# Performance work log

Hardware: AMD Instinct MI355X
Metric: run time of the kernel (lower is better)

The kernel has to match this reference:

```python
import jax, jax.numpy as jnp
import numpy as np

POOL = (4000, 4000, 4000)
N_GO = 12000
N_GENES = 20000
IN_F = 8
F = 64
B = 8
D_ATT = 5
L_DIM = 16
N_LAST = 4000
EPS = 1e-5


def _seg(v, ids, n):
    # v: [B, E, ...] -> segment-sum over axis 1
    return jax.vmap(lambda a: jax.ops.segment_sum(a, ids, num_segments=n))(v)


def _ln_nodes(x, g, b):
    # torch does LayerNorm(N) on x.permute(0,2,1): normalize over the NODE axis
    mu = x.mean(axis=1, keepdims=True)
    var = x.var(axis=1, keepdims=True)
    return (x - mu) * jax.lax.rsqrt(var + EPS) * g[None, :, None] + b[None, :, None]


def _bn(x, g, b):
    # BatchNorm1d, training-mode statistics (biased var); channel axis = 1
    if x.ndim == 2:
        mu = x.mean(axis=0)
        var = x.var(axis=0)
        return (x - mu) * jax.lax.rsqrt(var + EPS) * g + b
    mu = x.mean(axis=(0, 2), keepdims=True)
    var = x.var(axis=(0, 2), keepdims=True)
    return (x - mu) * jax.lax.rsqrt(var + EPS) * g[None, :, None] + b[None, :, None]


def _enc(x, src, dst, n, w_inc, w_s, w_att_in, w_att_s, g, b):
    x_in = x @ w_inc.T                 # [B,n,F]
    x_s = x @ w_s.T
    f1 = w_inc.shape[0]
    # W_att_in([x_src; x_dst]) == x_src @ W[:, :f1].T + x_dst @ W[:, f1:].T (GAT trick)
    a_src = x_in @ w_att_in[0, :f1]    # [B,n]
    a_dst = x_in @ w_att_in[0, f1:]
    v = jnp.exp(jnp.tanh(a_src[:, src] + a_dst[:, dst]))   # [B,E]
    vn = v / _seg(v, src, n)[:, src]                        # row-normalized attention
    x_incoming = _seg(vn[:, :, None] * x_in[:, dst, :], src, n)
    v_s = jax.nn.sigmoid(x_s @ w_att_s[0])                  # [B,n]
    out = x_incoming + x_s * v_s[:, :, None]
    return jax.nn.relu(_ln_nodes(out, g, b))


def _dec(x, src, dst, n_rows, offset, w_out, w_sout, g, b):
    x_out = x @ w_out.T
    x_s = x @ w_sout.T
    deg = jax.ops.segment_sum(jnp.ones(src.shape, x.dtype), src, num_segments=n_rows)
    v = 1.0 / deg[src]                                      # [E]
    x_outgoing = _seg(v[None, :, None] * x_out[:, dst, :], src, n_rows)
    out = x_outgoing.at[:, offset:, :].add(x_s)
    return jax.nn.relu(_ln_nodes(out, g, b))


def _forward(data, t, t_D,
             w_inc0, w_inc1, w_s0, w_s1, w_att_in0, w_att_in1, w_att_s0, w_att_s1,
             gb_g0, gb_b0, gb_g1, gb_b1,
             w_out0, w_out1, w_sout0, w_sout1,
             gbd_g0, gbd_b0, gbd_g1, gbd_b1,
             catt_w, catt_bn_g, catt_bn_b,
             conc_w, b_bn_g, b_bn_b,
             concd_w, bd_bn_g, bd_bn_b,
             lat_w1, lat_bn1_g, lat_bn1_b, lat_w2, lat_bn2_g, lat_bn2_b,
             Ag_row, Ag_col,
             enc_src0, enc_dst0, enc_src1, enc_dst1,
             dec_src0, dec_dst0, dec_src1, dec_dst1):
    # initial SNP->GO sparse embedding, one sparse matrix per input channel
    gathered = data[:, Ag_col]                         # [B,nnz]
    msg0 = gathered[:, :, None] * t.T[None, :, :]      # [B,nnz,IN_F]
    x = _seg(msg0, Ag_row, N_GO)                       # [B,N_GO,IN_F]

    # encoder (attention GCN + pooling)
    x = _enc(x, enc_src0, enc_dst0, N_GO, w_inc0, w_s0, w_att_in0, w_att_s0, gb_g0, gb_b0)
    x = x[:, POOL[0]:, :]
    x = _enc(x, enc_src1, enc_dst1, N_GO - POOL[0], w_inc1, w_s1, w_att_in1, w_att_s1, gb_g1, gb_b1)
    x = x[:, POOL[1]:, :]                              # [B,N_LAST,F]

    atten_out = jax.nn.relu(_bn(x @ catt_w.T, catt_bn_g, catt_bn_b))   # [B,N_LAST,D_ATT]
    inp_out = jax.nn.relu(_bn((x @ conc_w.T)[..., 0], b_bn_g, b_bn_b)) # [B,N_LAST]

    # decoder (degree-normalized unpooling)
    x = _dec(x, dec_src0, dec_dst0, POOL[1] + POOL[2], POOL[1], w_out0, w_sout0, gbd_g0, gbd_b0)
    x = _dec(x, dec_src1, dec_dst1, N_GO, POOL[0], w_out1, w_sout1, gbd_g1, gbd_b1)

    out_D = jax.nn.relu(_bn((x @ concd_w.T)[..., 0], bd_bn_g, bd_bn_b))  # [B,N_GO]
    x_D = _seg(out_D[:, Ag_row] * t_D[None, :], Ag_col, N_GENES)          # [B,N_GENES]

    h = jax.nn.relu(_bn(inp_out @ lat_w1.T, lat_bn1_g, lat_bn1_b))
    latent = jax.nn.relu(_bn(h @ lat_w2.T, lat_bn2_g, lat_bn2_b))         # [B,L_DIM]
    return latent, x_D, atten_out


def setup_inputs():
    rng = np.random.default_rng(0)
    # GO-GO adjacency edges (row-major unique, like coalesce)
    e = np.unique(rng.integers(0, N_GO, 144000).astype(np.int64) * N_GO
                  + rng.integers(0, N_GO, 144000))
    r = (e // N_GO).astype(np.int32)
    c = (e % N_GO).astype(np.int32)
    p0, p1 = POOL[0], POOL[0] + POOL[1]
    m = (r >= p0) & (c >= p0)
    enc_src1, enc_dst1 = r[m] - p0, c[m] - p0
    ti, tj = c, r                                  # edges of A.T
    m0 = (ti >= p0) & (tj >= p1)
    dec_src0, dec_dst0 = ti[m0] - p0, tj[m0] - p1
    m1 = tj >= p0
    dec_src1, dec_dst1 = ti[m1], tj[m1] - p0
    # gene <-> GO incidence
    eg = np.unique(rng.integers(0, N_GO, 240000).astype(np.int64) * N_GENES
                   + rng.integers(0, N_GENES, 240000))
    Ag_row = (eg // N_GENES).astype(np.int32)
    Ag_col = (eg % N_GENES).astype(np.int32)
    nnz = Ag_row.shape[0]

    ks = iter(jax.random.split(jax.random.key(0), 40))

    def nrm(shape, s=0.05):
        return jax.random.normal(next(ks), shape, jnp.float32) * s

    return {
        'data': nrm((B, N_GENES), 1.0),
        't': 1.0 + nrm((IN_F, nnz), 0.1),
        't_D': 1.0 + nrm((nnz,), 0.1),
        'w_inc0': nrm((F, IN_F)), 'w_inc1': nrm((F, F)),
        'w_s0': nrm((F, IN_F)), 'w_s1': nrm((F, F)),
        'w_att_in0': nrm((1, 2 * F)), 'w_att_in1': nrm((1, 2 * F)),
        'w_att_s0': nrm((1, F)), 'w_att_s1': nrm((1, F)),
        'gb_g0': jnp.ones(N_GO), 'gb_b0': jnp.zeros(N_GO),
        'gb_g1': jnp.ones(N_GO - p0), 'gb_b1': jnp.zeros(N_GO - p0),
        'w_out0': nrm((F, F)), 'w_out1': nrm((IN_F, F)),
        'w_sout0': nrm((F, F)), 'w_sout1': nrm((IN_F, F)),
        'gbd_g0': jnp.ones(POOL[1] + POOL[2]), 'gbd_b0': jnp.zeros(POOL[1] + POOL[2]),
        'gbd_g1': jnp.ones(N_GO), 'gbd_b1': jnp.zeros(N_GO),
        'catt_w': nrm((D_ATT, F)), 'catt_bn_g': jnp.ones(N_LAST), 'catt_bn_b': jnp.zeros(N_LAST),
        'conc_w': nrm((1, F)), 'b_bn_g': jnp.ones(N_LAST), 'b_bn_b': jnp.zeros(N_LAST),
        'concd_w': nrm((1, IN_F)), 'bd_bn_g': jnp.ones(N_GO), 'bd_bn_b': jnp.zeros(N_GO),
        'lat_w1': nrm((32, N_LAST)), 'lat_bn1_g': jnp.ones(32), 'lat_bn1_b': jnp.zeros(32),
        'lat_w2': nrm((L_DIM, 32)), 'lat_bn2_g': jnp.ones(L_DIM), 'lat_bn2_b': jnp.zeros(L_DIM),
        'Ag_row': jnp.asarray(Ag_row), 'Ag_col': jnp.asarray(Ag_col),
        'enc_src0': jnp.asarray(r), 'enc_dst0': jnp.asarray(c),
        'enc_src1': jnp.asarray(enc_src1), 'enc_dst1': jnp.asarray(enc_dst1),
        'dec_src0': jnp.asarray(dec_src0), 'dec_dst0': jnp.asarray(dec_dst0),
        'dec_src1': jnp.asarray(dec_src1), 'dec_dst1': jnp.asarray(dec_dst1),
    }


def reference(data, t, t_D,
              w_inc0, w_inc1, w_s0, w_s1, w_att_in0, w_att_in1, w_att_s0, w_att_s1,
              gb_g0, gb_b0, gb_g1, gb_b1,
              w_out0, w_out1, w_sout0, w_sout1,
              gbd_g0, gbd_b0, gbd_g1, gbd_b1,
              catt_w, catt_bn_g, catt_bn_b,
              conc_w, b_bn_g, b_bn_b,
              concd_w, bd_bn_g, bd_bn_b,
              lat_w1, lat_bn1_g, lat_bn1_b, lat_w2, lat_bn2_g, lat_bn2_b,
              Ag_row, Ag_col,
              enc_src0, enc_dst0, enc_src1, enc_dst1,
              dec_src0, dec_dst0, dec_src1, dec_dst1):
    return _forward(data, t, t_D,
                    w_inc0, w_inc1, w_s0, w_s1, w_att_in0, w_att_in1, w_att_s0, w_att_s1,
                    gb_g0, gb_b0, gb_g1, gb_b1,
                    w_out0, w_out1, w_sout0, w_sout1,
                    gbd_g0, gbd_b0, gbd_g1, gbd_b1,
                    catt_w, catt_bn_g, catt_bn_b,
                    conc_w, b_bn_g, b_bn_b,
                    concd_w, bd_bn_g, bd_bn_b,
                    lat_w1, lat_bn1_g, lat_bn1_b, lat_w2, lat_bn2_g, lat_bn2_b,
                    Ag_row, Ag_col,
                    enc_src0, enc_dst0, enc_src1, enc_dst1,
                    dec_src0, dec_dst0, dec_src1, dec_dst1)
```

## Files before the change

### kernel.cpp

```cpp
#include <hip/hip_runtime.h>
#include <math.h>

#define BB 8
#define N_GO 12000
#define N_GENES 20000
#define IN_F 8
#define FF 64
#define D_ATT 5
#define L_DIM 16
#define N_LAST 4000
#define P0_ 4000
#define EPSF 1e-5f

__global__ void k_bounds_bs(const int* __restrict__ src, int* __restrict__ rs,
                            int* __restrict__ re, int E, int n) {
    int r = blockIdx.x * 256 + threadIdx.x;
    if (r >= n) return;
    int lo = 0, hi = E;
    while (lo < hi) { int m = (lo + hi) >> 1; if (src[m] < r) lo = m + 1; else hi = m; }
    rs[r] = lo;
    int lo2 = lo, hi2 = E;
    while (lo2 < hi2) { int m = (lo2 + hi2) >> 1; if (src[m] < r + 1) lo2 = m + 1; else hi2 = m; }
    re[r] = lo2;
}

__global__ void k_tr_data(const float* __restrict__ data, float* __restrict__ dataT) {
    int idx = blockIdx.x * 256 + threadIdx.x;
    if (idx >= N_GENES * BB) return;
    int g = idx >> 3, b = idx & 7;
    dataT[idx] = data[b * N_GENES + g];
}

__global__ void k_gene2go_w(const float* __restrict__ dataT, const float* __restrict__ t,
                            const int* __restrict__ col, const int* __restrict__ rs,
                            const int* __restrict__ re, float* __restrict__ x0, int nnz) {
    int wid = blockIdx.x * 4 + (threadIdx.x >> 6);
    if (wid >= N_GO) return;
    int lane = threadIdx.x & 63;
    int f = lane & 7, eo = lane >> 3;
    int e0 = rs[wid], e1 = re[wid];
    float acc[BB];
#pragma unroll
    for (int b = 0; b < BB; b++) acc[b] = 0.f;
    for (int e = e0; e < e1; e += 8) {
        int ee = e + eo;
        bool ok = ee < e1;
        int ec = ok ? ee : (e1 - 1);
        int c = col[ec];
        float tv = ok ? t[(size_t)f * nnz + ee] : 0.f;
        const float4* dt = (const float4*)(dataT + (size_t)c * 8);
        float4 d0 = dt[0], d1 = dt[1];
        acc[0] += tv * d0.x; acc[1] += tv * d0.y; acc[2] += tv * d0.z; acc[3] += tv * d0.w;
        acc[4] += tv * d1.x; acc[5] += tv * d1.y; acc[6] += tv * d1.z; acc[7] += tv * d1.w;
    }
#pragma unroll
    for (int b = 0; b < BB; b++) {
        acc[b] += __shfl_xor(acc[b], 8);
        acc[b] += __shfl_xor(acc[b], 16);
        acc[b] += __shfl_xor(acc[b], 32);
    }
    if (lane < IN_F) {
#pragma unroll
        for (int b = 0; b < BB; b++)
            x0[((size_t)b * N_GO + wid) * IN_F + lane] = acc[b];
    }
}

template<bool SCAL>
__global__ __launch_bounds__(256, 2)
void k_linear2_att8(const float* __restrict__ X, const float* __restrict__ W1,
                    const float* __restrict__ W2, const float* __restrict__ watt,
                    const float* __restrict__ ws, float* __restrict__ Y1,
                    float* __restrict__ Y2, float* __restrict__ ASRC,
                    float* __restrict__ ADST,
                    int n_nodes, long xbs, int xoff, int total_waves) {
    __shared__ float w1s[IN_F * 65];
    __shared__ float w2s[IN_F * 65];
    int lane = threadIdx.x & 63;
    for (int i = threadIdx.x; i < IN_F * FF; i += 256) {
        int fo = i >> 3, k = i & 7;
        w1s[k * 65 + fo] = W1[i];
        w2s[k * 65 + fo] = W2[i];
    }
    __syncthreads();
    float w1r[IN_F], w2r[IN_F];
#pragma unroll
    for (int k = 0; k < IN_F; k++) {
        w1r[k] = w1s[k * 65 + lane];
        w2r[k] = w2s[k * 65 + lane];
        asm volatile("" : "+v"(w1r[k]));
        asm volatile("" : "+v"(w2r[k]));
    }
    float wa = 0.f, wb = 0.f, wc = 0.f;
    if (SCAL) { wa = watt[lane]; wb = watt[FF + lane]; wc = ws[lane]; }
    int wid = blockIdx.x * 4 + (threadIdx.x >> 6);
    for (int n = wid; n < n_nodes; n += total_waves) {
        for (int b = 0; b < BB; b++) {
            const float* xr = X + (size_t)b * xbs + (size_t)(n + xoff) * IN_F;
            float4 x0 = *(const float4*)xr, x1 = *(const float4*)(xr + 4);
            float a1 = x0.x * w1r[0] + x0.y * w1r[1] + x0.z * w1r[2] + x0.w * w1r[3]
                     + x1.x * w1r[4] + x1.y * w1r[5] + x1.z * w1r[6] + x1.w * w1r[7];
            float a2 = x0.x * w2r[0] + x0.y * w2r[1] + x0.z * w2r[2] + x0.w * w2r[3]
                     + x1.x * w2r[4] + x1.y * w2r[5] + x1.z * w2r[6] + x1.w * w2r[7];
            Y1[((size_t)b * n_nodes + n) * FF + lane] = a1;
            if (SCAL) {
                float s0 = a1 * wa, s1 = a1 * wb, s2 = a2 * wc;
                for (int m = 1; m < 64; m <<= 1) {
                    s0 += __shfl_xor(s0, m);
                    s1 += __shfl_xor(s1, m);
                    s2 += __shfl_xor(s2, m);
                }
                float vs = 1.f / (1.f + expf(-s2));
                Y2[((size_t)b * n_nodes + n) * FF + lane] = a2 * vs;
                if (lane == 0) {
                    ASRC[b * n_nodes + n] = s0;
                    ADST[b * n_nodes + n] = s1;
                }
            } else {
                Y2[((size_t)b * n_nodes + n) * FF + lane] = a2;
            }
        }
    }
}

template<bool SCAL>
__global__ __launch_bounds__(256, 1)
void k_lin64d(const float* __restrict__ X, const float* __restrict__ W1,
              const float* __restrict__ W2, const float* __restrict__ watt,
              const float* __restrict__ ws, float* __restrict__ Y1,
              float* __restrict__ Y2, float* __restrict__ ASRC,
              float* __restrict__ ADST,
              int n_nodes, long xbs, int xoff, int total_waves) {
    __shared__ float w1s[FF * 65];
    __shared__ float w2s[FF * 65];
    int lane = threadIdx.x & 63;
    for (int i = threadIdx.x; i < FF * FF; i += 256) {
        int fo = i >> 6, k = i & 63;
        w1s[fo * 65 + k] = W1[i];
        w2s[fo * 65 + k] = W2[i];
    }
    __syncthreads();
    float w1r[FF], w2r[FF];
#pragma unroll
    for (int k = 0; k < FF; k++) {
        w1r[k] = w1s[lane * 65 + k];
        w2r[k] = w2s[lane * 65 + k];
        asm volatile("" : "+v"(w1r[k]));
        asm volatile("" : "+v"(w2r[k]));
    }
    float wa = 0.f, wb = 0.f, wc = 0.f;
    if (SCAL) { wa = watt[lane]; wb = watt[FF + lane]; wc = ws[lane]; }
    int wid = blockIdx.x * 4 + (threadIdx.x >> 6);
    for (int n = wid; n < n_nodes; n += total_waves) {
        for (int b = 0; b < BB; b++) {
            const float* xr = X + (size_t)b * xbs + (size_t)(n + xoff) * FF;
            float a1 = 0.f, a2 = 0.f;
#pragma unroll
            for (int k = 0; k < FF; k += 4) {
                float4 x = *(const float4*)(xr + k);
                a1 += x.x * w1r[k] + x.y * w1r[k + 1] + x.z * w1r[k + 2] + x.w * w1r[k + 3];
                a2 += x.x * w2r[k] + x.y * w2r[k + 1] + x.z * w2r[k + 2] + x.w * w2r[k + 3];
            }
            Y1[((size_t)b * n_nodes + n) * FF + lane] = a1;
            if (SCAL) {
                float s0 = a1 * wa, s1 = a1 * wb, s2 = a2 * wc;
                for (int m = 1; m < 64; m <<= 1) {
                    s0 += __shfl_xor(s0, m);
                    s1 += __shfl_xor(s1, m);
                    s2 += __shfl_xor(s2, m);
                }
                float vs = 1.f / (1.f + expf(-s2));
                Y2[((size_t)b * n_nodes + n) * FF + lane] = a2 * vs;
                if (lane == 0) {
                    ASRC[b * n_nodes + n] = s0;
                    ADST[b * n_nodes + n] = s1;
                }
            } else {
                Y2[((size_t)b * n_nodes + n) * FF + lane] = a2;
            }
        }
    }
}

__global__ __launch_bounds__(256, 1)
void k_lin8d(const float* __restrict__ X, const float* __restrict__ W1,
             const float* __restrict__ W2, float* __restrict__ Y1,
             float* __restrict__ Y2, int n_nodes, long xbs, int xoff,
             int total_waves) {
    __shared__ float w1s[IN_F * 65];
    __shared__ float w2s[IN_F * 65];
    int lane = threadIdx.x & 63;
    for (int i = threadIdx.x; i < IN_F * FF; i += 256) {
        int fo = i >> 6, k = i & 63;
        w1s[fo * 65 + k] = W1[i];
        w2s[fo * 65 + k] = W2[i];
    }
    __syncthreads();
    int of = lane & 7;
    int slot = lane >> 3;
    float w1r[FF], w2r[FF];
#pragma unroll
    for (int k = 0; k < FF; k++) {
        w1r[k] = w1s[of * 65 + k];
        w2r[k] = w2s[of * 65 + k];
        asm volatile("" : "+v"(w1r[k]));
        asm volatile("" : "+v"(w2r[k]));
    }
    int wid = blockIdx.x * 4 + (threadIdx.x >> 6);
    for (long n0 = (long)wid * 8; n0 < n_nodes; n0 += (long)total_waves * 8) {
        int n = (int)n0 + slot;
        bool ok = (n < n_nodes);
        int nn = ok ? n : (n_nodes - 1);
        for (int b = 0; b < BB; b++) {
            const float* xr = X + (size_t)b * xbs + (size_t)(nn + xoff) * FF;
            float a1 = 0.f, a2 = 0.f;
#pragma unroll
            for (int k = 0; k < FF; k += 4) {
                float4 x = *(const float4*)(xr + k);
                a1 += x.x * w1r[k] + x.y * w1r[k + 1] + x.z * w1r[k + 2] + x.w * w1r[k + 3];
                a2 += x.x * w2r[k] + x.y * w2r[k + 1] + x.z * w2r[k + 2] + x.w * w2r[k + 3];
            }
            if (ok) {
                Y1[((size_t)b * n_nodes + n) * IN_F + of] = a1;
                Y2[((size_t)b * n_nodes + n) * IN_F + of] = a2;
            }
        }
    }
}

__global__ void k_edge_v(const float* __restrict__ a_src, const float* __restrict__ a_dst,
                         const int* __restrict__ src, const int* __restrict__ dst,
                         float* __restrict__ v, int E, int n_nodes) {
    int e = blockIdx.x * 256 + threadIdx.x;
    if (e >= E) return;
    int b = blockIdx.y;
    v[(size_t)b * E + e] = expf(tanhf(a_src[b * n_nodes + src[e]] + a_dst[b * n_nodes + dst[e]]));
}

__global__ void k_agg_enc_f(const float* __restrict__ Xin, const float* __restrict__ Xs,
                            const float* __restrict__ EDGEV,
                            const int* __restrict__ dst, const int* __restrict__ rs,
                            const int* __restrict__ re, float* __restrict__ Out,
                            float* __restrict__ sums, int n_nodes, int E, int nblk) {
    int b = blockIdx.x & 7;
    int wid = threadIdx.x >> 6;
    int lane = threadIdx.x & 63;
    const float* Xb  = Xin + (size_t)b * n_nodes * FF;
    const float* Xsb = Xs  + (size_t)b * n_nodes * FF;
    const float* vv  = EDGEV + (size_t)b * E;
    float s1 = 0.f, s2 = 0.f;
    for (int r = (blockIdx.x >> 3) * 4 + wid; r < n_nodes; r += nblk * 4) {
        int e0 = rs[r], e1 = re[r];
        float sv0 = 0.f, sv1 = 0.f, sv2 = 0.f, sv3 = 0.f;
        float acc0 = 0.f, acc1 = 0.f, acc2 = 0.f, acc3 = 0.f;
        int e = e0;
        for (; e + 3 < e1; e += 4) {
            int d0 = dst[e], d1 = dst[e + 1], d2 = dst[e + 2], d3 = dst[e + 3];
            float v0 = vv[e], v1 = vv[e + 1], v2 = vv[e + 2], v3 = vv[e + 3];
            sv0 += v0; sv1 += v1; sv2 += v2; sv3 += v3;
            acc0 += v0 * Xb[(size_t)d0 * FF + lane];
            acc1 += v1 * Xb[(size_t)d1 * FF + lane];
            acc2 += v2 * Xb[(size_t)d2 * FF + lane];
            acc3 += v3 * Xb[(size_t)d3 * FF + lane];
        }
        for (; e < e1; e++) {
            int d0 = dst[e];
            float v0 = vv[e];
            sv0 += v0;
            acc0 += v0 * Xb[(size_t)d0 * FF + lane];
        }
        float sv = (sv0 + sv1) + (sv2 + sv3);
        float acc = (acc0 + acc1) + (acc2 + acc3);
        float o = (e1 > e0) ? acc / sv : 0.f;
        o += Xsb[(size_t)r * FF + lane];
        Out[((size_t)b * n_nodes + r) * FF + lane] = o;
        s1 += o; s2 += o * o;
    }
    __shared__ float sh1[4][64], sh2[4][64];
    sh1[wid][lane] = s1; sh2[wid][lane] = s2;
    __syncthreads();
    if (wid == 0) {
        float a = sh1[0][lane] + sh1[1][lane] + sh1[2][lane] + sh1[3][lane];
        float c = sh2[0][lane] + sh2[1][lane] + sh2[2][lane] + sh2[3][lane];
        atomicAdd(&sums[(b * FF + lane) * 2],     a);
        atomicAdd(&sums[(b * FF + lane) * 2 + 1], c);
    }
}

__global__ void k_ln_stats(const float* __restrict__ X, float* __restrict__ sums,
                           int n_nodes, int Fdim, int npb) {
    int b = blockIdx.y;
    int f = threadIdx.x & (Fdim - 1);
    int nl = threadIdx.x / Fdim;
    int stride = 256 / Fdim;
    int n0 = blockIdx.x * npb;
    int n1 = n0 + npb; if (n1 > n_nodes) n1 = n_nodes;
    const float* xb = X + (size_t)b * n_nodes * Fdim;
    float s1 = 0.f, s2 = 0.f;
    for (int n = n0 + nl; n < n1; n += stride) {
        float x = xb[(size_t)n * Fdim + f];
        s1 += x; s2 += x * x;
    }
    __shared__ float sh1[256], sh2[256];
    sh1[threadIdx.x] = s1; sh2[threadIdx.x] = s2;
    __syncthreads();
    for (int o = 128; o >= Fdim; o >>= 1) {
        if (threadIdx.x < o) { sh1[threadIdx.x] += sh1[threadIdx.x + o]; sh2[threadIdx.x] += sh2[threadIdx.x + o]; }
        __syncthreads();
    }
    if (threadIdx.x < Fdim) {
        atomicAdd(&sums[(b * Fdim + threadIdx.x) * 2],     sh1[threadIdx.x]);
        atomicAdd(&sums[(b * Fdim + threadIdx.x) * 2 + 1], sh2[threadIdx.x]);
    }
}

__global__ void k_ln_apply_relu(const float* __restrict__ X, const float* __restrict__ sums,
                                const float* __restrict__ g, const float* __restrict__ bb,
                                float* __restrict__ Y, int n_nodes, int Fdim) {
    long idx = (long)blockIdx.x * 256 + threadIdx.x;
    if (idx >= (long)n_nodes * Fdim) return;
    int b = blockIdx.y;
    int n = (int)(idx / Fdim);
    int f = (int)(idx % Fdim);
    float s1 = sums[(b * Fdim + f) * 2], s2 = sums[(b * Fdim + f) * 2 + 1];
    float mu = s1 / n_nodes;
    float var = s2 / n_nodes - mu * mu;
    float rs = rsqrtf(var + EPSF);
    size_t o = (size_t)b * n_nodes * Fdim + idx;
    float y = (X[o] - mu) * rs * g[n] + bb[n];
    Y[o] = fmaxf(y, 0.f);
}

__global__ void k_deg_i(const int* __restrict__ src, int* __restrict__ deg, int E) {
    int e = blockIdx.x * 256 + threadIdx.x;
    if (e < E) atomicAdd(&deg[src[e]], 1);
}

__global__ void k_scan(const int* __restrict__ deg, int* __restrict__ rsd,
                       int* __restrict__ cursor, int n) {
    __shared__ int part[1024];
    int t = threadIdx.x;
    int chunk = (n + 1023) >> 10;
    int s0 = t * chunk, s1 = s0 + chunk; if (s1 > n) s1 = n;
    int s = 0;
    for (int i = s0; i < s1 && i < n; i++) s += deg[i];
    part[t] = s;
    __syncthreads();
    for (int o = 1; o < 1024; o <<= 1) {
        int v = (t >= o) ? part[t - o] : 0;
        __syncthreads();
        part[t] += v;
        __syncthreads();
    }
    int base = (t == 0) ? 0 : part[t - 1];
    for (int i = s0; i < s1 && i < n; i++) {
        rsd[i] = base; cursor[i] = base;
        base += deg[i];
    }
    if (t == 1023) rsd[n] = part[1023];
}

__global__ void k_scatter(const int* __restrict__ src, const int* __restrict__ dst,
                          int* __restrict__ cursor, int* __restrict__ csrd, int E) {
    int e = blockIdx.x * 256 + threadIdx.x;
    if (e >= E) return;
    int pos = atomicAdd(&cursor[src[e]], 1);
    csrd[pos] = dst[e];
}

__global__ void k_scatter2(const int* __restrict__ key, const int* __restrict__ row,
                           const float* __restrict__ tD, int* __restrict__ cursor,
                           int* __restrict__ csrr, float* __restrict__ csrt, int E) {
    int e = blockIdx.x * 256 + threadIdx.x;
    if (e >= E) return;
    int pos = atomicAdd(&cursor[key[e]], 1);
    csrr[pos] = row[e];
    csrt[pos] = tD[e];
}

__global__ void k_xd_g(const float* __restrict__ outD, const int* __restrict__ rsg,
                       const int* __restrict__ csrr, const float* __restrict__ csrt,
                       float* __restrict__ xD) {
    int g = blockIdx.x * 4 + (threadIdx.x >> 6);
    if (g >= N_GENES) return;
    int lane = threadIdx.x & 63;
    int b = lane & 7, slot = lane >> 3;
    int e0 = rsg[g], e1 = rsg[g + 1];
    float acc = 0.f;
    for (int e = e0 + slot; e < e1; e += 8)
        acc += csrt[e] * outD[(size_t)b * N_GO + csrr[e]];
    acc += __shfl_xor(acc, 8);
    acc += __shfl_xor(acc, 16);
    acc += __shfl_xor(acc, 32);
    if (lane < BB)
        xD[(size_t)b * N_GENES + g] = acc;
}

__global__ void k_agg_dec64(const float* __restrict__ Xout, const float* __restrict__ Xs,
                            const int* __restrict__ rsd, const int* __restrict__ csrd,
                            float* __restrict__ Out, float* __restrict__ sums,
                            int n_rows, int n_in, int offset, int nblk) {
    int b = blockIdx.x & 7;
    int wid = threadIdx.x >> 6;
    int lane = threadIdx.x & 63;
    const float* Xb = Xout + (size_t)b * n_in * FF;
    int nxs = n_rows - offset;
    const float* Xsb = Xs + (size_t)b * nxs * FF;
    float s1 = 0.f, s2 = 0.f;
    for (int r = (blockIdx.x >> 3) * 4 + wid; r < n_rows; r += nblk * 4) {
        int e0 = rsd[r], e1 = rsd[r + 1];
        float acc0 = 0.f, acc1 = 0.f, acc2 = 0.f, acc3 = 0.f;
        int e = e0;
        for (; e + 3 < e1; e += 4) {
            acc0 += Xb[(size_t)csrd[e] * FF + lane];
            acc1 += Xb[(size_t)csrd[e + 1] * FF + lane];
            acc2 += Xb[(size_t)csrd[e + 2] * FF + lane];
            acc3 += Xb[(size_t)csrd[e + 3] * FF + lane];
        }
        for (; e < e1; e++) acc0 += Xb[(size_t)csrd[e] * FF + lane];
        float acc = (acc0 + acc1) + (acc2 + acc3);
        float o = (e1 > e0) ? acc / (float)(e1 - e0) : 0.f;
        if (r >= offset)
            o += Xsb[(size_t)(r - offset) * FF + lane];
        Out[((size_t)b * n_rows + r) * FF + lane] = o;
        s1 += o; s2 += o * o;
    }
    __shared__ float sh1[4][64], sh2[4][64];
    sh1[wid][lane] = s1; sh2[wid][lane] = s2;
    __syncthreads();
    if (wid == 0) {
        float a = sh1[0][lane] + sh1[1][lane] + sh1[2][lane] + sh1[3][lane];
        float c = sh2[0][lane] + sh2[1][lane] + sh2[2][lane] + sh2[3][lane];
        atomicAdd(&sums[(b * FF + lane) * 2],     a);
        atomicAdd(&sums[(b * FF + lane) * 2 + 1], c);
    }
}

__global__ void k_agg_dec8(const float* __restrict__ Xout, const float* __restrict__ Xs,
                           const int* __restrict__ rsd, const int* __restrict__ csrd,
                           float* __restrict__ Out, int n_rows, int n_in, int offset) {
    int r = blockIdx.x * 4 + (threadIdx.x >> 6);
    if (r >= n_rows) return;
    int lane = threadIdx.x & 63;
    int f = lane & 7, slot = lane >> 3;
    int e0 = rsd[r], e1 = rsd[r + 1];
    float acc[BB];
#pragma unroll
    for (int b = 0; b < BB; b++) acc[b] = 0.f;
    for (int e = e0 + slot; e < e1; e += 8) {
        int d = csrd[e];
#pragma unroll
        for (int b = 0; b < BB; b++)
            acc[b] += Xout[((size_t)b * n_in + d) * IN_F + f];
    }
#pragma unroll
    for (int b = 0; b < BB; b++) {
        acc[b] += __shfl_xor(acc[b], 8);
        acc[b] += __shfl_xor(acc[b], 16);
        acc[b] += __shfl_xor(acc[b], 32);
    }
    float coef = (e1 > e0) ? 1.f / (float)(e1 - e0) : 0.f;
    int nxs = n_rows - offset;
    if (lane < IN_F) {
#pragma unroll
        for (int b = 0; b < BB; b++) {
            float o = acc[b] * coef;
            if (r >= offset)
                o += Xs[((size_t)b * nxs + (r - offset)) * IN_F + lane];
            Out[((size_t)b * n_rows + r) * IN_F + lane] = o;
        }
    }
}

__global__ void k_heads(const float* __restrict__ X, const float* __restrict__ Wa,
                        const float* __restrict__ wc, const float* __restrict__ ga,
                        const float* __restrict__ ba, const float* __restrict__ gc,
                        const float* __restrict__ bc, float* __restrict__ ATT,
                        float* __restrict__ INP, long xbs, int xoff) {
    int i = blockIdx.x * 4 + (threadIdx.x >> 6);
    if (i >= N_LAST) return;
    int lane = threadIdx.x & 63;
    float w0 = Wa[0 * FF + lane], w1 = Wa[1 * FF + lane], w2 = Wa[2 * FF + lane];
    float w3 = Wa[3 * FF + lane], w4 = Wa[4 * FF + lane];
    float wcv = wc[lane];
    float y[BB][D_ATT], yc[BB];
    float s1 = 0.f, s2 = 0.f;
#pragma unroll
    for (int b = 0; b < BB; b++) {
        float x = X[(size_t)b * xbs + (size_t)(i + xoff) * FF + lane];
        float p0 = x * w0, p1 = x * w1, p2 = x * w2, p3 = x * w3, p4 = x * w4, pc = x * wcv;
        for (int m = 1; m < 64; m <<= 1) {
            p0 += __shfl_xor(p0, m); p1 += __shfl_xor(p1, m); p2 += __shfl_xor(p2, m);
            p3 += __shfl_xor(p3, m); p4 += __shfl_xor(p4, m); pc += __shfl_xor(pc, m);
        }
        y[b][0] = p0; y[b][1] = p1; y[b][2] = p2; y[b][3] = p3; y[b][4] = p4;
        yc[b] = pc;
        s1 += p0 + p1 + p2 + p3 + p4;
        s2 += p0 * p0 + p1 * p1 + p2 * p2 + p3 * p3 + p4 * p4;
    }
    const float cnt = (float)(BB * D_ATT);
    float mu = s1 / cnt, var = s2 / cnt - mu * mu;
    float rsv = rsqrtf(var + EPSF);
    float gg = ga[i], bv = ba[i];
#pragma unroll
    for (int b = 0; b < BB; b++) {
        float yv = lane == 0 ? y[b][0] : lane == 1 ? y[b][1] : lane == 2 ? y[b][2]
                 : lane == 3 ? y[b][3] : y[b][4];
        if (lane < D_ATT)
            ATT[((size_t)b * N_LAST + i) * D_ATT + lane] = fmaxf((yv - mu) * rsv * gg + bv, 0.f);
    }
    float c1 = 0.f, c2 = 0.f;
#pragma unroll
    for (int b = 0; b < BB; b++) { c1 += yc[b]; c2 += yc[b] * yc[b]; }
    float muc = c1 / BB, varc = c2 / BB - muc * muc;
    float rc = rsqrtf(varc + EPSF);
    float ggc = gc[i], bvc = bc[i];
    if (lane < BB) {
        float v = lane == 0 ? yc[0] : lane == 1 ? yc[1] : lane == 2 ? yc[2] : lane == 3 ? yc[3]
                : lane == 4 ? yc[4] : lane == 5 ? yc[5] : lane == 6 ? yc[6] : yc[7];
        INP[(size_t)lane * N_LAST + i] = fmaxf((v - muc) * rc * ggc + bvc, 0.f);
    }
}

template<int FIN>
__global__ void k_head_scalar(const float* __restrict__ X, const float* __restrict__ w,
                              const float* __restrict__ g, const float* __restrict__ bb,
                              float* __restrict__ Z, int n_nodes, long xbs, int xoff) {
    int i = blockIdx.x * 256 + threadIdx.x;
    if (i >= n_nodes) return;
    float y[BB];
    float s1 = 0.f, s2 = 0.f;
    const float4* wr = (const float4*)w;
    for (int b = 0; b < BB; b++) {
        const float4* xr = (const float4*)(X + (size_t)b * xbs + (size_t)(i + xoff) * FIN);
        float acc = 0.f;
#pragma unroll
        for (int q = 0; q < FIN / 4; q++) {
            float4 x = xr[q], u = wr[q];
            acc += x.x * u.x + x.y * u.y + x.z * u.z + x.w * u.w;
        }
        y[b] = acc; s1 += acc; s2 += acc * acc;
    }
    float mu = s1 / BB, var = s2 / BB - mu * mu;
    float rs = rsqrtf(var + EPSF);
    float gg = g[i], bv = bb[i];
    for (int b = 0; b < BB; b++)
        Z[(size_t)b * n_nodes + i] = fmaxf((y[b] - mu) * rs * gg + bv, 0.f);
}

__global__ void k_lat1(const float* __restrict__ INP, const float* __restrict__ W,
                       const float* __restrict__ g, const float* __restrict__ bb,
                       float* __restrict__ H1R) {
    int j = blockIdx.x;
    int w = threadIdx.x >> 6;
    int lane = threadIdx.x & 63;
    const float* xr = INP + (size_t)w * N_LAST;
    const float* wr = W + (size_t)j * N_LAST;
    float s = 0.f;
    for (int k = lane; k < N_LAST; k += 64) s += xr[k] * wr[k];
    for (int o = 32; o > 0; o >>= 1) s += __shfl_down(s, o);
    __shared__ float sh[BB];
    if (lane == 0) sh[w] = s;
    __syncthreads();
    if (threadIdx.x < BB) {
        float s1 = 0.f, s2 = 0.f;
        for (int q = 0; q < BB; q++) { float y = sh[q]; s1 += y; s2 += y * y; }
        float mu = s1 / BB, var = s2 / BB - mu * mu;
        float rs = rsqrtf(var + EPSF);
        H1R[threadIdx.x * 32 + j] = fmaxf((sh[threadIdx.x] - mu) * rs * g[j] + bb[j], 0.f);
    }
}

__global__ void k_lat2(const float* __restrict__ H1R, const float* __restrict__ W2,
                       const float* __restrict__ g, const float* __restrict__ bb,
                       float* __restrict__ out_lat) {
    int b = threadIdx.x >> 4, j = threadIdx.x & 15;
    float acc = 0.f;
    for (int k = 0; k < 32; k++) acc += H1R[b * 32 + k] * W2[j * 32 + k];
    __shared__ float sh[128];
    sh[threadIdx.x] = acc;
    __syncthreads();
    float s1 = 0.f, s2 = 0.f;
    for (int q = 0; q < BB; q++) { float y = sh[q * 16 + j]; s1 += y; s2 += y * y; }
    float mu = s1 / BB, var = s2 / BB - mu * mu;
    float rs = rsqrtf(var + EPSF);
    out_lat[b * 16 + j] = fmaxf((acc - mu) * rs * g[j] + bb[j], 0.f);
}

extern "C" void kernel_launch(void* const* d_in, const int* in_sizes, int n_in,
                              void* d_out, int out_size, void* d_ws, size_t ws_size,
                              hipStream_t stream) {
    const float* data      = (const float*)d_in[0];
    const float* t         = (const float*)d_in[1];
    const float* t_D       = (const float*)d_in[2];
    const float* w_inc0    = (const float*)d_in[3];
    const float* w_inc1    = (const float*)d_in[4];
    const float* w_s0      = (const float*)d_in[5];
    const float* w_s1      = (const float*)d_in[6];
    const float* w_att_in0 = (const float*)d_in[7];
    const float* w_att_in1 = (const float*)d_in[8];
    const float* w_att_s0  = (const float*)d_in[9];
    const float* w_att_s1  = (const float*)d_in[10];
    const float* gb_g0     = (const float*)d_in[11];
    const float* gb_b0     = (const float*)d_in[12];
    const float* gb_g1     = (const float*)d_in[13];
    const float* gb_b1     = (const float*)d_in[14];
    const float* w_out0    = (const float*)d_in[15];
    const float* w_out1    = (const float*)d_in[16];
    const float* w_sout0   = (const float*)d_in[17];
    const float* w_sout1   = (const float*)d_in[18];
    const float* gbd_g0    = (const float*)d_in[19];
    const float* gbd_b0    = (const float*)d_in[20];
    const float* gbd_g1    = (const float*)d_in[21];
    const float* gbd_b1    = (const float*)d_in[22];
    const float* catt_w    = (const float*)d_in[23];
    const float* catt_bn_g = (const float*)d_in[24];
    const float* catt_bn_b = (const float*)d_in[25];
    const float* conc_w    = (const float*)d_in[26];
    const float* b_bn_g    = (const float*)d_in[27];
    const float* b_bn_b    = (const float*)d_in[28];
    const float* concd_w   = (const float*)d_in[29];
    const float* bd_bn_g   = (const float*)d_in[30];
    const float* bd_bn_b   = (const float*)d_in[31];
    const float* lat_w1    = (const float*)d_in[32];
    const float* lat_bn1_g = (const float*)d_in[33];
    const float* lat_bn1_b = (const float*)d_in[34];
    const float* lat_w2    = (const float*)d_in[35];
    const float* lat_bn2_g = (const float*)d_in[36];
    const float* lat_bn2_b = (const float*)d_in[37];
    const int* Ag_row   = (const int*)d_in[38];
    const int* Ag_col   = (const int*)d_in[39];
    const int* enc_src0 = (const int*)d_in[40];
    const int* enc_dst0 = (const int*)d_in[41];
    const int* enc_src1 = (const int*)d_in[42];
    const int* enc_dst1 = (const int*)d_in[43];
    const int* dec_src0 = (const int*)d_in[44];
    const int* dec_dst0 = (const int*)d_in[45];
    const int* dec_src1 = (const int*)d_in[46];
    const int* dec_dst1 = (const int*)d_in[47];

    const int nnz = in_sizes[2];
    const int E0  = in_sizes[40];
    const int E1  = in_sizes[42];
    const int ED0 = in_sizes[44];
    const int ED1 = in_sizes[46];
    int EDMAX = (ED0 > ED1 ? ED0 : ED1);
    if (nnz > EDMAX) EDMAX = nnz;

    char* wsb = (char*)d_ws;
    size_t off = 0;
    auto alloc = [&](size_t bytes) -> void* {
        void* p = wsb + off;
        off += (bytes + 255) & ~(size_t)255;
        return p;
    };
    const size_t ARENA = (size_t)BB * N_GO * FF;
    float* P0 = (float*)alloc(ARENA * 4);
    float* P1 = (float*)alloc(ARENA * 4);
    float* P2 = (float*)alloc(ARENA * 4);
    float* P3 = (float*)alloc(ARENA * 4);
    float* EDGEV = (float*)alloc((size_t)BB * E0 * 4);
    float* ASRC = (float*)alloc((size_t)BB * N_GO * 4);
    float* ADST = (float*)alloc((size_t)BB * N_GO * 4);
    float* SUMS = (float*)alloc(2 * BB * FF * 4);
    float* INP  = (float*)alloc((size_t)BB * N_LAST * 4);
    float* OUTD = (float*)alloc((size_t)BB * N_GO * 4);
    float* H1R  = (float*)alloc(BB * 32 * 4);
    float* DATAT = (float*)alloc((size_t)N_GENES * BB * 4);
    int* RS   = (int*)alloc(N_GO * 4);
    int* RE   = (int*)alloc(N_GO * 4);
    int* DEGI = (int*)alloc(N_GENES * 4);
    int* RSD  = (int*)alloc((N_GENES + 1) * 4);
    int* CURS = (int*)alloc(N_GENES * 4);
    int* CSRD = (int*)alloc((size_t)EDMAX * 4);
    float* CSRT = (float*)alloc((size_t)nnz * 4);

    float* out_lat = (float*)d_out;
    float* out_xd  = out_lat + BB * L_DIM;
    float* out_att = out_xd + (size_t)BB * N_GENES;

    dim3 blk(256);
    auto g1 = [](long n) { return dim3((unsigned)((n + 255) / 256)); };
    auto g2 = [](long n, int y) { return dim3((unsigned)((n + 255) / 256), (unsigned)y); };
    auto gw = [](int n) { return dim3((unsigned)((n + 3) / 4)); };
    const int LNB = 1024;
    const int LWAVES = LNB * 4;
    const int ANB = 256;
    const int N1 = N_GO - P0_;

    k_tr_data<<<g1(N_GENES * BB), blk, 0, stream>>>(data, DATAT);
    k_bounds_bs<<<g1(N_GO), blk, 0, stream>>>(Ag_row, RS, RE, nnz, N_GO);
    k_gene2go_w<<<gw(N_GO), blk, 0, stream>>>(DATAT, t, Ag_col, RS, RE, P0, nnz);

    k_linear2_att8<true><<<dim3(LNB), blk, 0, stream>>>(P0, w_inc0, w_s0, w_att_in0, w_att_s0,
        P1, P2, ASRC, ADST, N_GO, (long)N_GO * IN_F, 0, LWAVES);
    k_bounds_bs<<<g1(N_GO), blk, 0, stream>>>(enc_src0, RS, RE, E0, N_GO);
    k_edge_v<<<g2(E0, BB), blk, 0, stream>>>(ASRC, ADST, enc_src0, enc_dst0, EDGEV, E0, N_GO);
    hipMemsetAsync(SUMS, 0, 2 * BB * FF * 4, stream);
    k_agg_enc_f<<<dim3(ANB * 8), blk, 0, stream>>>(P1, P2, EDGEV, enc_dst0, RS, RE, P3, SUMS, N_GO, E0, ANB);
    k_ln_apply_relu<<<g2((long)N_GO * FF, BB), blk, 0, stream>>>(P3, SUMS, gb_g0, gb_b0, P0, N_GO, FF);

    k_lin64d<true><<<dim3(LNB), blk, 0, stream>>>(P0, w_inc1, w_s1, w_att_in1, w_att_s1,
        P1, P2, ASRC, ADST, N1, (long)N_GO * FF, P0_, LWAVES);
    k_bounds_bs<<<g1(N1), blk, 0, stream>>>(enc_src1, RS, RE, E1, N1);
    k_edge_v<<<g2(E1, BB), blk, 0, stream>>>(ASRC, ADST, enc_src1, enc_dst1, EDGEV, E1, N1);
    hipMemsetAsync(SUMS, 0, 2 * BB * FF * 4, stream);
    k_agg_enc_f<<<dim3(ANB * 8), blk, 0, stream>>>(P1, P2, EDGEV, enc_dst1, RS, RE, P3, SUMS, N1, E1, ANB);
    k_ln_apply_relu<<<g2((long)N1 * FF, BB), blk, 0, stream>>>(P3, SUMS, gb_g1, gb_b1, P0, N1, FF);

    k_heads<<<gw(N_LAST), blk, 0, stream>>>(P0, catt_w, conc_w, catt_bn_g, catt_bn_b,
                                            b_bn_g, b_bn_b, out_att, INP, (long)N1 * FF, P0_);

    k_lin64d<false><<<dim3(LNB), blk, 0, stream>>>(P0, w_out0, w_sout0, nullptr, nullptr,
        P1, P2, nullptr, nullptr, N_LAST, (long)N1 * FF, P0_, LWAVES);
    hipMemsetAsync(DEGI, 0, 8000 * 4, stream);
    k_deg_i<<<g1(ED0), blk, 0, stream>>>(dec_src0, DEGI, ED0);
    k_scan<<<dim3(1), dim3(1024), 0, stream>>>(DEGI, RSD, CURS, 8000);
    k_scatter<<<g1(ED0), blk, 0, stream>>>(dec_src0, dec_dst0, CURS, CSRD, ED0);
    hipMemsetAsync(SUMS, 0, 2 * BB * FF * 4, stream);
    k_agg_dec64<<<dim3(ANB * 8), blk, 0, stream>>>(P1, P2, RSD, CSRD, P3, SUMS, 8000, N_LAST, 4000, ANB);
    k_ln_apply_relu<<<g2((long)8000 * FF, BB), blk, 0, stream>>>(P3, SUMS, gbd_g0, gbd_b0, P0, 8000, FF);

    k_lin8d<<<dim3(LNB), blk, 0, stream>>>(P0, w_out1, w_sout1, P1, P2, 8000, (long)8000 * FF, 0, LWAVES);
    hipMemsetAsync(DEGI, 0, N_GO * 4, stream);
    k_deg_i<<<g1(ED1), blk, 0, stream>>>(dec_src1, DEGI, ED1);
    k_scan<<<dim3(1), dim3(1024), 0, stream>>>(DEGI, RSD, CURS, N_GO);
    k_scatter<<<g1(ED1), blk, 0, stream>>>(dec_src1, dec_dst1, CURS, CSRD, ED1);
    k_agg_dec8<<<gw(N_GO), blk, 0, stream>>>(P1, P2, RSD, CSRD, P3, N_GO, 8000, 4000);
    hipMemsetAsync(SUMS, 0, 2 * BB * IN_F * 4, stream);
    k_ln_stats<<<dim3((N_GO + 511) / 512, BB), blk, 0, stream>>>(P3, SUMS, N_GO, IN_F, 512);
    k_ln_apply_relu<<<g2((long)N_GO * IN_F, BB), blk, 0, stream>>>(P3, SUMS, gbd_g1, gbd_b1, P0, N_GO, IN_F);

    k_head_scalar<IN_F><<<g1(N_GO), blk, 0, stream>>>(P0, concd_w, bd_bn_g, bd_bn_b, OUTD, N_GO, (long)N_GO * IN_F, 0);
    hipMemsetAsync(DEGI, 0, N_GENES * 4, stream);
    k_deg_i<<<g1(nnz), blk, 0, stream>>>(Ag_col, DEGI, nnz);
    k_scan<<<dim3(1), dim3(1024), 0, stream>>>(DEGI, RSD, CURS, N_GENES);
    k_scatter2<<<g1(nnz), blk, 0, stream>>>(Ag_col, Ag_row, t_D, CURS, CSRD, CSRT, nnz);
    k_xd_g<<<gw(N_GENES), blk, 0, stream>>>(OUTD, RSD, CSRD, CSRT, out_xd);

    k_lat1<<<dim3(32), dim3(512), 0, stream>>>(INP, lat_w1, lat_bn1_g, lat_bn1_b, H1R);
    k_lat2<<<dim3(1), dim3(128), 0, stream>>>(H1R, lat_w2, lat_bn2_g, lat_bn2_b, out_lat);

    (void)n_in; (void)out_size; (void)ws_size;
}
```

Baseline: 523.8 us.

## Restructure 64-wide linear kernel to stream weights from LDS with multi-node tiles

Replaces the register-resident 64x64 weight copies of the 64-feature linear kernel with transposed shared-memory weights read per k-group. Each wave now handles four nodes at once and each block only two batch entries, using a 2D grid. The goal is to cut register pressure so occupancy rises (launch bounds allow 4 blocks), and to reuse each weight load across four nodes. The cost is extra LDS traffic, and the x reads are now strided across four rows with no tail guard on the loads.

```diff
diff --git a/kernel.cpp b/kernel.cpp
--- a/kernel.cpp
+++ b/kernel.cpp
@@ -124,59 +124,72 @@
 }
 
 template<bool SCAL>
-__global__ __launch_bounds__(256, 1)
-void k_lin64d(const float* __restrict__ X, const float* __restrict__ W1,
+__global__ __launch_bounds__(256, 4)
+void k_lin64m(const float* __restrict__ X, const float* __restrict__ W1,
               const float* __restrict__ W2, const float* __restrict__ watt,
               const float* __restrict__ ws, float* __restrict__ Y1,
               float* __restrict__ Y2, float* __restrict__ ASRC,
               float* __restrict__ ADST,
-              int n_nodes, long xbs, int xoff, int total_waves) {
+              int n_nodes, long xbs, int xoff, int ngroups) {
     __shared__ float w1s[FF * 65];
     __shared__ float w2s[FF * 65];
     int lane = threadIdx.x & 63;
     for (int i = threadIdx.x; i < FF * FF; i += 256) {
         int fo = i >> 6, k = i & 63;
-        w1s[fo * 65 + k] = W1[i];
-        w2s[fo * 65 + k] = W2[i];
-    }
-    __syncthreads();
-    float w1r[FF], w2r[FF];
-#pragma unroll
-    for (int k = 0; k < FF; k++) {
-        w1r[k] = w1s[lane * 65 + k];
-        w2r[k] = w2s[lane * 65 + k];
-        asm volatile("" : "+v"(w1r[k]));
-        asm volatile("" : "+v"(w2r[k]));
-    }
+        w1s[k * 65 + fo] = W1[i];
+        w2s[k * 65 + fo] = W2[i];
+    }
+    __syncthreads();
     float wa = 0.f, wb = 0.f, wc = 0.f;
     if (SCAL) { wa = watt[lane]; wb = watt[FF + lane]; wc = ws[lane]; }
     int wid = blockIdx.x * 4 + (threadIdx.x >> 6);
-    for (int n = wid; n < n_nodes; n += total_waves) {
-        for (int b = 0; b < BB; b++) {
-            const float* xr = X + (size_t)b * xbs + (size_t)(n + xoff) * FF;
-            float a1 = 0.f, a2 = 0.f;
-#pragma unroll
-            for (int k = 0; k < FF; k += 4) {
-                float4 x = *(const float4*)(xr + k);
-                a1 += x.x * w1r[k] + x.y * w1r[k + 1] + x.z * w1r[k + 2] + x.w * w1r[k + 3];
-                a2 += x.x * w2r[k] + x.y * w2r[k + 1] + x.z * w2r[k + 2] + x.w * w2r[k + 3];
+    int b0 = blockIdx.y * 2;
+    for (int g = wid; g < ngroups; g += gridDim.x * 4) {
+        int n0 = g * 4;
+        for (int bi = 0; bi < 2; bi++) {
+            int b = b0 + bi;
+            const float* xr = X + (size_t)b * xbs + (size_t)(n0 + xoff) * FF;
+            float a1[4] = {0.f, 0.f, 0.f, 0.f};
+            float a2[4] = {0.f, 0.f, 0.f, 0.f};
+            for (int kg = 0; kg < 16; kg++) {
+                int k = kg * 4;
+                float w10 = w1s[(k + 0) * 65 + lane];
+                float w11 = w1s[(k + 1) * 65 + lane];
+                float w12 = w1s[(k + 2) * 65 + lane];
+                float w13 = w1s[(k + 3) * 65 + lane];
+                float w20 = w2s[(k + 0) * 65 + lane];
+                float w21 = w2s[(k + 1) * 65 + lane];
+                float w22 = w2s[(k + 2) * 65 + lane];
+                float w23 = w2s[(k + 3) * 65 + lane];
+#pragma unroll
+                for (int j = 0; j < 4; j++) {
+                    float4 x = *(const float4*)(xr + (size_t)j * FF + k);
+                    a1[j] += x.x * w10 + x.y * w11 + x.z * w12 + x.w * w13;
+                    a2[j] += x.x * w20 + x.y * w21 + x.z * w22 + x.w * w23;
+                }
             }
-            Y1[((size_t)b * n_nodes + n) * FF + lane] = a1;
-            if (SCAL) {
-                float s0 = a1 * wa, s1 = a1 * wb, s2 = a2 * wc;
-                for (int m = 1; m < 64; m <<= 1) {
-                    s0 += __shfl_xor(s0, m);
-                    s1 += __shfl_xor(s1, m);
-                    s2 += __shfl_xor(s2, m);
+#pragma unroll
+            for (int j = 0; j < 4; j++) {
+                int n = n0 + j;
+                if (n < n_nodes) {
+                    Y1[((size_t)b * n_nodes + n) * FF + lane] = a1[j];
+                    if (SCAL) {
+                        float s0 = a1[j] * wa, s1 = a1[j] * wb, s2 = a2[j] * wc;
+                        for (int m = 1; m < 64; m <<= 1) {
+                            s0 += __shfl_xor(s0, m);
+                            s1 += __shfl_xor(s1, m);
+                            s2 += __shfl_xor(s2, m);
+                        }
+                        float vs = 1.f / (1.f + expf(-s2));
+                        Y2[((size_t)b * n_nodes + n) * FF + lane] = a2[j] * vs;
+                        if (lane == 0) {
+                            ASRC[b * n_nodes + n] = s0;
+                            ADST[b * n_nodes + n] = s1;
+                        }
+                    } else {
+                        Y2[((size_t)b * n_nodes + n) * FF + lane] = a2[j];
+                    }
                 }
-                float vs = 1.f / (1.f + expf(-s2));
-                Y2[((size_t)b * n_nodes + n) * FF + lane] = a2 * vs;
-                if (lane == 0) {
-                    ASRC[b * n_nodes + n] = s0;
-                    ADST[b * n_nodes + n] = s1;
-                }
-            } else {
-                Y2[((size_t)b * n_nodes + n) * FF + lane] = a2;
             }
         }
     }
@@ -700,8 +713,11 @@
     k_agg_enc_f<<<dim3(ANB * 8), blk, 0, stream>>>(P1, P2, EDGEV, enc_dst0, RS, RE, P3, SUMS, N_GO, E0, ANB);
     k_ln_apply_relu<<<g2((long)N_GO * FF, BB), blk, 0, stream>>>(P3, SUMS, gb_g0, gb_b0, P0, N_GO, FF);
 
-    k_lin64d<true><<<dim3(LNB), blk, 0, stream>>>(P0, w_inc1, w_s1, w_att_in1, w_att_s1,
-        P1, P2, ASRC, ADST, N1, (long)N_GO * FF, P0_, LWAVES);
+    {
+        int ng = (N1 + 3) / 4;
+        k_lin64m<true><<<dim3((ng + 3) / 4, 4), blk, 0, stream>>>(P0, w_inc1, w_s1, w_att_in1, w_att_s1,
+            P1, P2, ASRC, ADST, N1, (long)N_GO * FF, P0_, ng);
+    }
     k_bounds_bs<<<g1(N1), blk, 0, stream>>>(enc_src1, RS, RE, E1, N1);
     k_edge_v<<<g2(E1, BB), blk, 0, stream>>>(ASRC, ADST, enc_src1, enc_dst1, EDGEV, E1, N1);
     hipMemsetAsync(SUMS, 0, 2 * BB * FF * 4, stream);
@@ -711,8 +727,11 @@
     k_heads<<<gw(N_LAST), blk, 0, stream>>>(P0, catt_w, conc_w, catt_bn_g, catt_bn_b,
                                             b_bn_g, b_bn_b, out_att, INP, (long)N1 * FF, P0_);
 
-    k_lin64d<false><<<dim3(LNB), blk, 0, stream>>>(P0, w_out0, w_sout0, nullptr, nullptr,
-        P1, P2, nullptr, nullptr, N_LAST, (long)N1 * FF, P0_, LWAVES);
+    {
+        int ng = (N_LAST + 3) / 4;
+        k_lin64m<false><<<dim3((ng + 3) / 4, 4), blk, 0, stream>>>(P0, w_out0, w_sout0, nullptr, nullptr,
+            P1, P2, nullptr, nullptr, N_LAST, (long)N1 * FF, P0_, ng);
+    }
     hipMemsetAsync(DEGI, 0, 8000 * 4, stream);
     k_deg_i<<<g1(ED0), blk, 0, stream>>>(dec_src0, DEGI, ED0);
     k_scan<<<dim3(1), dim3(1024), 0, stream>>>(DEGI, RSD, CURS, 8000);
```

Result: slower. 882.3 us (+68.5%).
